# Optimization experiments

Hardware: AMD Instinct MI355X
Metric: run time of the kernel (lower is better)

The kernel has to match this reference:

```python
import jax, jax.numpy as jnp
import numpy as np

N = 50000
E = 800000
DIM = 128


def setup_inputs() -> dict:
    key = jax.random.key(0)
    ks = jax.random.split(key, 12)
    s = 1.0 / np.sqrt(DIM)
    s2 = 1.0 / np.sqrt(2 * DIM)
    return {
        "h": jax.random.normal(ks[0], (N, DIM), dtype=jnp.float32),
        "edge_index": jax.random.randint(ks[1], (2, E), 0, N, dtype=jnp.int64),
        # msg_mlp: Linear(dim,dim) -> ReLU -> Linear(dim,dim) -> ReLU
        "W1": jax.random.uniform(ks[2], (DIM, DIM), jnp.float32, -s, s),
        "b1": jax.random.uniform(ks[3], (DIM,), jnp.float32, -s, s),
        "W2": jax.random.uniform(ks[4], (DIM, DIM), jnp.float32, -s, s),
        "b2": jax.random.uniform(ks[5], (DIM,), jnp.float32, -s, s),
        # update_mlp: Linear(2*dim,dim) -> ReLU -> Linear(dim,dim)
        "U1": jax.random.uniform(ks[6], (2 * DIM, DIM), jnp.float32, -s2, s2),
        "c1": jax.random.uniform(ks[7], (DIM,), jnp.float32, -s2, s2),
        "U2": jax.random.uniform(ks[8], (DIM, DIM), jnp.float32, -s, s),
        "c2": jax.random.uniform(ks[9], (DIM,), jnp.float32, -s, s),
    }


def reference(h, edge_index, W1, b1, W2, b2, U1, c1, U2, c2):
    row, col = edge_index[0], edge_index[1]
    # gather source features and run message MLP on edges: [E, dim]
    x = h[col]
    m = jax.nn.relu(x @ W1 + b1)
    m = jax.nn.relu(m @ W2 + b2)
    # scatter-add messages to destination nodes: [N, dim]
    agg = jax.ops.segment_sum(m, row, num_segments=h.shape[0])
    # degree normalization (bincount of row, clamped at 1)
    deg = jax.ops.segment_sum(jnp.ones((m.shape[0],), m.dtype), row, num_segments=h.shape[0])
    deg = jnp.maximum(deg, 1.0)[:, None]
    agg = agg / deg
    # update MLP on [h, agg]
    z = jnp.concatenate([h, agg], axis=1)
    z = jax.nn.relu(z @ U1 + c1)
    return z @ U2 + c2
```

## Files before the change

### kernel.cpp

```cpp
#include <hip/hip_runtime.h>
#include <cstddef>

#define NN 50000
#define EE 800000
#define DIM 128
#define CAP 128

#define PREP_BLKS 320
#define ZERO_BLKS 49
#define EDGE_BLKS 3125
#define MLP_BLKS  782
#define GUP_BLKS  3125

typedef __attribute__((ext_vector_type(8))) short bf16x8;
typedef __attribute__((ext_vector_type(4))) float f32x4;

__device__ __forceinline__ unsigned short f2bf(float x) {
    unsigned u = __float_as_uint(x);
    unsigned r = (u + 0x7FFFu + ((u >> 16) & 1u)) >> 16;
    return (unsigned short)r;
}

__device__ __forceinline__ float bf2f(unsigned short b) {
    return __uint_as_float((unsigned)b << 16);
}

__device__ __forceinline__ int load_idx(const void* ei, bool i64, long long i) {
    return i64 ? (int)((const long long*)ei)[i] : ((const int*)ei)[i];
}

__device__ __forceinline__ bool detect_i64_inline(const void* ei) {
    int l = threadIdx.x & 63;
    int v = ((const int*)ei)[2 * l + 1];
    return __ballot(v != 0) == 0ULL;
}

__global__ __launch_bounds__(256) void prep_zero_kernel(
    const float* __restrict__ W1, const float* __restrict__ W2,
    const float* __restrict__ U1, const float* __restrict__ U2,
    unsigned short* __restrict__ W1t, unsigned short* __restrict__ W2t,
    unsigned short* __restrict__ U1h, unsigned short* __restrict__ U1l,
    unsigned short* __restrict__ U2h, unsigned short* __restrict__ U2l,
    int* __restrict__ cnt)
{
    int bid = blockIdx.x;
    if (bid < PREP_BLKS) {
        int idx = bid * 256 + threadIdx.x;
        if (idx < 32768) {
            int m   = idx >> 14;
            int rem = idx & 16383;
            int n = rem >> 7, k = rem & 127;
            const float* W = m ? W2 : W1;
            unsigned short* Wt = m ? W2t : W1t;
            Wt[n * DIM + k] = f2bf(W[k * DIM + n]);
        } else if (idx < 65536) {
            int r = idx - 32768;
            int k = r >> 7, n = r & 127;
            float w = U1[r];
            unsigned short hx = f2bf(w);
            U1h[n * 256 + k] = hx;
            U1l[n * 256 + k] = f2bf(w - bf2f(hx));
        } else {
            int r = idx - 65536;
            int k = r >> 7, n = r & 127;
            float w = U2[r];
            unsigned short hx = f2bf(w);
            U2h[n * 128 + k] = hx;
            U2l[n * 128 + k] = f2bf(w - bf2f(hx));
        }
    } else {
        int base = (bid - PREP_BLKS) * 1024 + threadIdx.x * 4;
        if (base + 4 <= NN) {
            *(int4*)(cnt + base) = (int4){0, 0, 0, 0};
        } else {
            #pragma unroll
            for (int k = 0; k < 4; ++k)
                if (base + k < NN) cnt[base + k] = 0;
        }
    }
}

__global__ __launch_bounds__(256) void bucket_mlp_kernel(
    const void* __restrict__ ei, const float* __restrict__ h,
    const unsigned short* __restrict__ W1t, const float* __restrict__ b1,
    const unsigned short* __restrict__ W2t, const float* __restrict__ b2,
    int* __restrict__ cnt, int* __restrict__ bucket,
    unsigned short* __restrict__ Mh)
{
    __shared__ unsigned short xs[4][16][136];

    if (blockIdx.x < EDGE_BLKS) {
        bool i64 = detect_i64_inline(ei);
        int e = blockIdx.x * 256 + threadIdx.x;
        if (e < EE) {
            int r = load_idx(ei, i64, e);
            int c = load_idx(ei, i64, (long long)EE + e);
            int slot = atomicAdd(&cnt[r], 1);
            if (slot < CAP) bucket[r * CAP + slot] = c;
        }
        return;
    }

    const int tid  = threadIdx.x;
    const int lane = tid & 63;
    const int wid  = tid >> 6;
    const int g    = lane >> 4;
    const int c    = lane & 15;
    const int half = lane >> 5;
    const int hl   = lane & 31;
    const int nbase = (blockIdx.x - EDGE_BLKS) * 64 + wid * 16;

    #pragma unroll
    for (int e = 0; e < 16; e += 2) {
        int n = nbase + e + half;
        int nc = n < NN ? n : NN - 1;
        float4 v = *(const float4*)(h + (size_t)nc * DIM + hl * 4);
        unsigned short h0 = f2bf(v.x), h1 = f2bf(v.y), h2 = f2bf(v.z), h3 = f2bf(v.w);
        *(uint2*)&xs[wid][e + half][hl * 4] =
            (uint2){(unsigned)h0 | ((unsigned)h1 << 16), (unsigned)h2 | ((unsigned)h3 << 16)};
    }

    bf16x8 a[4];
    #pragma unroll
    for (int s = 0; s < 4; ++s)
        a[s] = *(const bf16x8*)&xs[wid][c][s * 32 + g * 8];

    f32x4 acc[8];
    #pragma unroll
    for (int t = 0; t < 8; ++t) {
        float bv = b1[t * 16 + c];
        acc[t] = (f32x4){bv, bv, bv, bv};
    }
    #pragma unroll
    for (int t = 0; t < 8; ++t) {
        #pragma unroll
        for (int s = 0; s < 4; ++s) {
            bf16x8 bf = *(const bf16x8*)&W1t[(t * 16 + c) * DIM + s * 32 + g * 8];
            acc[t] = __builtin_amdgcn_mfma_f32_16x16x32_bf16(a[s], bf, acc[t], 0, 0, 0);
        }
    }
    #pragma unroll
    for (int t = 0; t < 8; ++t)
        #pragma unroll
        for (int j = 0; j < 4; ++j)
            xs[wid][g * 4 + j][t * 16 + c] = f2bf(fmaxf(acc[t][j], 0.f));

    #pragma unroll
    for (int s = 0; s < 4; ++s)
        a[s] = *(const bf16x8*)&xs[wid][c][s * 32 + g * 8];

    #pragma unroll
    for (int t = 0; t < 8; ++t) {
        float bv = b2[t * 16 + c];
        acc[t] = (f32x4){bv, bv, bv, bv};
    }
    #pragma unroll
    for (int t = 0; t < 8; ++t) {
        #pragma unroll
        for (int s = 0; s < 4; ++s) {
            bf16x8 bf = *(const bf16x8*)&W2t[(t * 16 + c) * DIM + s * 32 + g * 8];
            acc[t] = __builtin_amdgcn_mfma_f32_16x16x32_bf16(a[s], bf, acc[t], 0, 0, 0);
        }
    }

    #pragma unroll
    for (int t = 0; t < 8; ++t)
        #pragma unroll
        for (int j = 0; j < 4; ++j)
            xs[wid][g * 4 + j][t * 16 + c] = f2bf(fmaxf(acc[t][j], 0.f));

    #pragma unroll
    for (int e = 0; e < 16; ++e) {
        int n = nbase + e;
        if (n < NN)
            *(unsigned*)(Mh + (size_t)n * DIM + lane * 2) = *(const unsigned*)&xs[wid][e][lane * 2];
    }
}

__global__ __launch_bounds__(256, 8) void gup4_kernel(
    const float* __restrict__ h,
    const unsigned short* __restrict__ Mh, const int* __restrict__ bucket,
    const int* __restrict__ cnt,
    const unsigned short* __restrict__ U1h, const unsigned short* __restrict__ U1l,
    const unsigned short* __restrict__ U2h, const unsigned short* __restrict__ U2l,
    const float* __restrict__ c1, const float* __restrict__ c2,
    float* __restrict__ out)
{
    __shared__ unsigned short xa[2][16][136];
    __shared__ unsigned short xh[2][16][136];
    const int tid  = threadIdx.x;
    const int lane = tid & 63;
    const int wid  = tid >> 6;
    const int g    = lane >> 4;
    const int c    = lane & 15;
    const int half = lane >> 5;
    const int hl   = lane & 31;
    const int nbase = blockIdx.x * 16;

    #pragma unroll 1
    for (int pass = 0; pass < 2; ++pass) {
        int r  = 4 * wid + 2 * pass + half;
        int n  = nbase + r;
        int d  = cnt[n];
        int dg = d < CAP ? d : CAP;
        const int* brow = bucket + (size_t)n * CAP;
        float s0 = 0.f, s1 = 0.f, s2 = 0.f, s3 = 0.f;
        #pragma unroll 1
        for (int base = 0; base < dg; base += 32) {
            int m = dg - base; if (m > 32) m = 32;
            int idx = (hl < m) ? brow[base + hl] : 0;
            int j = 0;
            for (; j + 8 <= m; j += 8) {
                uint2 u[8];
                #pragma unroll
                for (int k = 0; k < 8; ++k) {
                    int si = __shfl(idx, (half << 5) + j + k);
                    u[k] = *(const uint2*)(Mh + (size_t)si * DIM + hl * 4);
                }
                #pragma unroll
                for (int k = 0; k < 8; ++k) {
                    s0 += __uint_as_float(u[k].x << 16);
                    s1 += __uint_as_float(u[k].x & 0xFFFF0000u);
                    s2 += __uint_as_float(u[k].y << 16);
                    s3 += __uint_as_float(u[k].y & 0xFFFF0000u);
                }
            }
            for (; j < m; ++j) {
                int si = __shfl(idx, (half << 5) + j);
                uint2 u0 = *(const uint2*)(Mh + (size_t)si * DIM + hl * 4);
                s0 += __uint_as_float(u0.x << 16);
                s1 += __uint_as_float(u0.x & 0xFFFF0000u);
                s2 += __uint_as_float(u0.y << 16);
                s3 += __uint_as_float(u0.y & 0xFFFF0000u);
            }
        }
        float inv = 1.0f / fmaxf((float)d, 1.0f);
        s0 *= inv; s1 *= inv; s2 *= inv; s3 *= inv;
        unsigned short h0 = f2bf(s0), h1 = f2bf(s1), h2 = f2bf(s2), h3 = f2bf(s3);
        unsigned short l0 = f2bf(s0 - bf2f(h0)), l1 = f2bf(s1 - bf2f(h1));
        unsigned short l2 = f2bf(s2 - bf2f(h2)), l3 = f2bf(s3 - bf2f(h3));
        *(uint2*)&xa[0][r][hl * 4] =
            (uint2){(unsigned)h0 | ((unsigned)h1 << 16), (unsigned)h2 | ((unsigned)h3 << 16)};
        *(uint2*)&xa[1][r][hl * 4] =
            (uint2){(unsigned)l0 | ((unsigned)l1 << 16), (unsigned)l2 | ((unsigned)l3 << 16)};

        float4 v = *(const float4*)(h + (size_t)n * DIM + hl * 4);
        unsigned short p0 = f2bf(v.x), p1 = f2bf(v.y), p2 = f2bf(v.z), p3 = f2bf(v.w);
        unsigned short q0 = f2bf(v.x - bf2f(p0)), q1 = f2bf(v.y - bf2f(p1));
        unsigned short q2 = f2bf(v.z - bf2f(p2)), q3 = f2bf(v.w - bf2f(p3));
        *(uint2*)&xh[0][r][hl * 4] =
            (uint2){(unsigned)p0 | ((unsigned)p1 << 16), (unsigned)p2 | ((unsigned)p3 << 16)};
        *(uint2*)&xh[1][r][hl * 4] =
            (uint2){(unsigned)q0 | ((unsigned)q1 << 16), (unsigned)q2 | ((unsigned)q3 << 16)};
    }
    __syncthreads();

    f32x4 acc[2];
    #pragma unroll
    for (int tt = 0; tt < 2; ++tt) {
        int t = 2 * wid + tt;
        float bv = c1[t * 16 + c];
        acc[tt] = (f32x4){bv, bv, bv, bv};
    }
    {
        bf16x8 ah[4], al[4];
        #pragma unroll
        for (int s = 0; s < 4; ++s) {
            ah[s] = *(const bf16x8*)&xa[0][c][s * 32 + g * 8];
            al[s] = *(const bf16x8*)&xa[1][c][s * 32 + g * 8];
        }
        #pragma unroll
        for (int tt = 0; tt < 2; ++tt) {
            int t = 2 * wid + tt;
            #pragma unroll
            for (int s = 0; s < 4; ++s) {
                int kof = 128 + s * 32 + g * 8;
                bf16x8 bh = *(const bf16x8*)&U1h[(t * 16 + c) * 256 + kof];
                bf16x8 bl = *(const bf16x8*)&U1l[(t * 16 + c) * 256 + kof];
                acc[tt] = __builtin_amdgcn_mfma_f32_16x16x32_bf16(ah[s], bh, acc[tt], 0, 0, 0);
                acc[tt] = __builtin_amdgcn_mfma_f32_16x16x32_bf16(al[s], bh, acc[tt], 0, 0, 0);
                acc[tt] = __builtin_amdgcn_mfma_f32_16x16x32_bf16(ah[s], bl, acc[tt], 0, 0, 0);
            }
        }
        #pragma unroll
        for (int s = 0; s < 4; ++s) {
            ah[s] = *(const bf16x8*)&xh[0][c][s * 32 + g * 8];
            al[s] = *(const bf16x8*)&xh[1][c][s * 32 + g * 8];
        }
        #pragma unroll
        for (int tt = 0; tt < 2; ++tt) {
            int t = 2 * wid + tt;
            #pragma unroll
            for (int s = 0; s < 4; ++s) {
                int kof = s * 32 + g * 8;
                bf16x8 bh = *(const bf16x8*)&U1h[(t * 16 + c) * 256 + kof];
                bf16x8 bl = *(const bf16x8*)&U1l[(t * 16 + c) * 256 + kof];
                acc[tt] = __builtin_amdgcn_mfma_f32_16x16x32_bf16(ah[s], bh, acc[tt], 0, 0, 0);
                acc[tt] = __builtin_amdgcn_mfma_f32_16x16x32_bf16(al[s], bh, acc[tt], 0, 0, 0);
                acc[tt] = __builtin_amdgcn_mfma_f32_16x16x32_bf16(ah[s], bl, acc[tt], 0, 0, 0);
            }
        }
    }
    __syncthreads();

    #pragma unroll
    for (int tt = 0; tt < 2; ++tt) {
        int t = 2 * wid + tt;
        #pragma unroll
        for (int j = 0; j < 4; ++j) {
            float yv = fmaxf(acc[tt][j], 0.f);
            unsigned short hx = f2bf(yv);
            xh[0][g * 4 + j][t * 16 + c] = hx;
            xh[1][g * 4 + j][t * 16 + c] = f2bf(yv - bf2f(hx));
        }
    }
    __syncthreads();

    bf16x8 yh[4], yl[4];
    #pragma unroll
    for (int s = 0; s < 4; ++s) {
        yh[s] = *(const bf16x8*)&xh[0][c][s * 32 + g * 8];
        yl[s] = *(const bf16x8*)&xh[1][c][s * 32 + g * 8];
    }
    f32x4 acc2[2];
    #pragma unroll
    for (int tt = 0; tt < 2; ++tt) {
        int t = 2 * wid + tt;
        float bv = c2[t * 16 + c];
        acc2[tt] = (f32x4){bv, bv, bv, bv};
    }
    #pragma unroll
    for (int tt = 0; tt < 2; ++tt) {
        int t = 2 * wid + tt;
        #pragma unroll
        for (int s = 0; s < 4; ++s) {
            int kof = s * 32 + g * 8;
            bf16x8 bh = *(const bf16x8*)&U2h[(t * 16 + c) * 128 + kof];
            bf16x8 bl = *(const bf16x8*)&U2l[(t * 16 + c) * 128 + kof];
            acc2[tt] = __builtin_amdgcn_mfma_f32_16x16x32_bf16(yh[s], bh, acc2[tt], 0, 0, 0);
            acc2[tt] = __builtin_amdgcn_mfma_f32_16x16x32_bf16(yl[s], bh, acc2[tt], 0, 0, 0);
            acc2[tt] = __builtin_amdgcn_mfma_f32_16x16x32_bf16(yh[s], bl, acc2[tt], 0, 0, 0);
        }
    }

    #pragma unroll
    for (int tt = 0; tt < 2; ++tt) {
        int t = 2 * wid + tt;
        #pragma unroll
        for (int j = 0; j < 4; ++j) {
            int n = nbase + g * 4 + j;
            out[(size_t)n * DIM + t * 16 + c] = acc2[tt][j];
        }
    }
}

__global__ void detect_i64_kernel(const int* __restrict__ ei, int* __restrict__ flag) {
    int l = threadIdx.x;
    int v = ei[2 * l + 1];
    unsigned long long b = __ballot(v != 0);
    if (l == 0) flag[0] = (b == 0ULL) ? 1 : 0;
}

__global__ __launch_bounds__(256) void prep_w_kernel(
    const float* __restrict__ W1, const float* __restrict__ W2,
    unsigned short* __restrict__ W1t, unsigned short* __restrict__ W2t)
{
    int idx = blockIdx.x * 256 + threadIdx.x;
    int m   = idx >> 14;
    int rem = idx & 16383;
    int n = rem >> 7, k = rem & 127;
    const float* W = m ? W2 : W1;
    unsigned short* Wt = m ? W2t : W1t;
    Wt[n * DIM + k] = f2bf(W[k * DIM + n]);
}

__global__ __launch_bounds__(256) void deg_i_kernel(const void* __restrict__ ei,
                                                    const int* __restrict__ flag,
                                                    int* __restrict__ deg) {
    bool i64 = flag[0] != 0;
    int e = blockIdx.x * 256 + threadIdx.x;
    if (e < EE) {
        int r = load_idx(ei, i64, e);
        atomicAdd(&deg[r], 1);
    }
}

__global__ __launch_bounds__(256) void msg_kernel(
    const float* __restrict__ h, const void* __restrict__ ei, const int* __restrict__ flag,
    const unsigned short* __restrict__ W1t, const float* __restrict__ b1,
    const unsigned short* __restrict__ W2t, const float* __restrict__ b2,
    float* __restrict__ agg)
{
    __shared__ unsigned short xs[4][16][136];
    const int tid  = threadIdx.x;
    const int lane = tid & 63;
    const int wid  = tid >> 6;
    const int g    = lane >> 4;
    const int c    = lane & 15;
    const bool i64 = flag[0] != 0;
    const int ebase = blockIdx.x * 64 + wid * 16;

    #pragma unroll
    for (int e = 0; e < 16; ++e) {
        int src = load_idx(ei, i64, (long long)EE + (ebase + e));
        float2 v = *(const float2*)(h + (size_t)src * DIM + lane * 2);
        unsigned p = (unsigned)f2bf(v.x) | ((unsigned)f2bf(v.y) << 16);
        *(unsigned*)&xs[wid][e][lane * 2] = p;
    }
    __syncthreads();

    bf16x8 a[4];
    #pragma unroll
    for (int s = 0; s < 4; ++s)
        a[s] = *(const bf16x8*)&xs[wid][c][s * 32 + g * 8];

    f32x4 acc[8];
    #pragma unroll
    for (int t = 0; t < 8; ++t) {
        float bv = b1[t * 16 + c];
        acc[t] = (f32x4){bv, bv, bv, bv};
    }
    #pragma unroll
    for (int t = 0; t < 8; ++t) {
        #pragma unroll
        for (int s = 0; s < 4; ++s) {
            bf16x8 bf = *(const bf16x8*)&W1t[(t * 16 + c) * DIM + s * 32 + g * 8];
            acc[t] = __builtin_amdgcn_mfma_f32_16x16x32_bf16(a[s], bf, acc[t], 0, 0, 0);
        }
    }
    __syncthreads();
    #pragma unroll
    for (int t = 0; t < 8; ++t)
        #pragma unroll
        for (int j = 0; j < 4; ++j)
            xs[wid][g * 4 + j][t * 16 + c] = f2bf(fmaxf(acc[t][j], 0.f));
    __syncthreads();

    #pragma unroll
    for (int s = 0; s < 4; ++s)
        a[s] = *(const bf16x8*)&xs[wid][c][s * 32 + g * 8];

    #pragma unroll
    for (int t = 0; t < 8; ++t) {
        float bv = b2[t * 16 + c];
        acc[t] = (f32x4){bv, bv, bv, bv};
    }
    #pragma unroll
    for (int t = 0; t < 8; ++t) {
        #pragma unroll
        for (int s = 0; s < 4; ++s) {
            bf16x8 bf = *(const bf16x8*)&W2t[(t * 16 + c) * DIM + s * 32 + g * 8];
            acc[t] = __builtin_amdgcn_mfma_f32_16x16x32_bf16(a[s], bf, acc[t], 0, 0, 0);
        }
    }

    #pragma unroll
    for (int j = 0; j < 4; ++j) {
        int r = load_idx(ei, i64, ebase + g * 4 + j);
        #pragma unroll
        for (int t = 0; t < 8; ++t)
            atomicAdd(&agg[(size_t)r * DIM + t * 16 + c], fmaxf(acc[t][j], 0.f));
    }
}

__global__ __launch_bounds__(256) void upd_kernel(
    const float* __restrict__ h, const float* __restrict__ aggout,
    const int* __restrict__ deg,
    const float* __restrict__ U1, const float* __restrict__ c1,
    const float* __restrict__ U2, const float* __restrict__ c2,
    float* __restrict__ out)
{
    __shared__ float zs[4][8][2 * DIM];
    const int tid  = threadIdx.x;
    const int lane = tid & 63;
    const int wid  = tid >> 6;
    const int nbase = blockIdx.x * 32 + wid * 8;

    #pragma unroll
    for (int i = 0; i < 8; ++i) {
        int n = nbase + i;
        if (n < NN) {
            float2 hv = *(const float2*)(h + (size_t)n * DIM + lane * 2);
            *(float2*)&zs[wid][i][lane * 2] = hv;
            float d = fmaxf((float)deg[n], 1.0f);
            float inv = 1.0f / d;
            float2 av = *(const float2*)(aggout + (size_t)n * DIM + lane * 2);
            av.x *= inv; av.y *= inv;
            *(float2*)&zs[wid][i][DIM + lane * 2] = av;
        }
    }
    __syncthreads();

    float acc0[8], acc1[8];
    {
        float cc0 = c1[lane], cc1 = c1[lane + 64];
        #pragma unroll
        for (int i = 0; i < 8; ++i) { acc0[i] = cc0; acc1[i] = cc1; }
    }
    for (int k = 0; k < 2 * DIM; k += 4) {
        float wa[4], wb[4];
        #pragma unroll
        for (int kk = 0; kk < 4; ++kk) {
            wa[kk] = U1[(k + kk) * DIM + lane];
            wb[kk] = U1[(k + kk) * DIM + lane + 64];
        }
        #pragma unroll
        for (int i = 0; i < 8; ++i) {
            float4 zv = *(const float4*)&zs[wid][i][k];
            acc0[i] = fmaf(zv.x, wa[0], acc0[i]);
            acc1[i] = fmaf(zv.x, wb[0], acc1[i]);
            acc0[i] = fmaf(zv.y, wa[1], acc0[i]);
            acc1[i] = fmaf(zv.y, wb[1], acc1[i]);
            acc0[i] = fmaf(zv.z, wa[2], acc0[i]);
            acc1[i] = fmaf(zv.z, wb[2], acc1[i]);
            acc0[i] = fmaf(zv.w, wa[3], acc0[i]);
            acc1[i] = fmaf(zv.w, wb[3], acc1[i]);
        }
    }
    __syncthreads();
    #pragma unroll
    for (int i = 0; i < 8; ++i) {
        zs[wid][i][lane]      = fmaxf(acc0[i], 0.f);
        zs[wid][i][lane + 64] = fmaxf(acc1[i], 0.f);
    }
    __syncthreads();

    {
        float cc0 = c2[lane], cc1 = c2[lane + 64];
        #pragma unroll
        for (int i = 0; i < 8; ++i) { acc0[i] = cc0; acc1[i] = cc1; }
    }
    for (int k = 0; k < DIM; k += 4) {
        float wa[4], wb[4];
        #pragma unroll
        for (int kk = 0; kk < 4; ++kk) {
            wa[kk] = U2[(k + kk) * DIM + lane];
            wb[kk] = U2[(k + kk) * DIM + lane + 64];
        }
        #pragma unroll
        for (int i = 0; i < 8; ++i) {
            float4 zv = *(const float4*)&zs[wid][i][k];
            acc0[i] = fmaf(zv.x, wa[0], acc0[i]);
            acc1[i] = fmaf(zv.x, wb[0], acc1[i]);
            acc0[i] = fmaf(zv.y, wa[1], acc0[i]);
            acc1[i] = fmaf(zv.y, wb[1], acc1[i]);
            acc0[i] = fmaf(zv.z, wa[2], acc0[i]);
            acc1[i] = fmaf(zv.z, wb[2], acc1[i]);
            acc0[i] = fmaf(zv.w, wa[3], acc0[i]);
            acc1[i] = fmaf(zv.w, wb[3], acc1[i]);
        }
    }

    #pragma unroll
    for (int i = 0; i < 8; ++i) {
        int n = nbase + i;
        if (n < NN) {
            out[(size_t)n * DIM + lane]      = acc0[i];
            out[(size_t)n * DIM + lane + 64] = acc1[i];
        }
    }
}

extern "C" void kernel_launch(void* const* d_in, const int* in_sizes, int n_in,
                              void* d_out, int out_size, void* d_ws, size_t ws_size,
                              hipStream_t stream) {
    const float* h  = (const float*)d_in[0];
    const void*  ei = d_in[1];
    const float* W1 = (const float*)d_in[2];
    const float* b1 = (const float*)d_in[3];
    const float* W2 = (const float*)d_in[4];
    const float* b2 = (const float*)d_in[5];
    const float* U1 = (const float*)d_in[6];
    const float* c1 = (const float*)d_in[7];
    const float* U2 = (const float*)d_in[8];
    const float* c2 = (const float*)d_in[9];
    float* out = (float*)d_out;

    const size_t BIG_BYTES = 38862144;
    const bool big = ws_size >= BIG_BYTES;

    char* wsb = (char*)d_ws;
    unsigned short *Mh, *W1t, *W2t, *U1h, *U1l, *U2h, *U2l;
    int *bucket, *cnt, *flag;
    if (big) {
        Mh     = (unsigned short*)wsb;
        bucket = (int*)(wsb + 12800000);
        cnt    = (int*)(wsb + 38400000);
        flag   = nullptr;
        W1t    = (unsigned short*)(wsb + 38600000);
        W2t    = (unsigned short*)(wsb + 38632768);
        U1h    = (unsigned short*)(wsb + 38665536);
        U1l    = (unsigned short*)(wsb + 38731072);
        U2h    = (unsigned short*)(wsb + 38796608);
        U2l    = (unsigned short*)(wsb + 38829376);
    } else {
        Mh     = nullptr; bucket = nullptr;
        U1h = U1l = U2h = U2l = nullptr;
        cnt    = (int*)wsb;
        flag   = (int*)(wsb + 200000);
        W1t    = (unsigned short*)(wsb + 200064);
        W2t    = (unsigned short*)(wsb + 200064 + 32768);
    }

    if (big) {
        prep_zero_kernel<<<PREP_BLKS + ZERO_BLKS, 256, 0, stream>>>(
            W1, W2, U1, U2, W1t, W2t, U1h, U1l, U2h, U2l, cnt);
        bucket_mlp_kernel<<<EDGE_BLKS + MLP_BLKS, 256, 0, stream>>>(
            ei, h, W1t, b1, W2t, b2, cnt, bucket, Mh);
        gup4_kernel<<<GUP_BLKS, 256, 0, stream>>>(h, Mh, bucket, cnt,
                                                  U1h, U1l, U2h, U2l, c1, c2, out);
    } else {
        detect_i64_kernel<<<1, 64, 0, stream>>>((const int*)ei, flag);
        prep_w_kernel<<<128, 256, 0, stream>>>(W1, W2, W1t, W2t);
        hipMemsetAsync(cnt, 0, (size_t)NN * sizeof(int), stream);
        deg_i_kernel<<<(EE + 255) / 256, 256, 0, stream>>>(ei, flag, cnt);
        hipMemsetAsync(d_out, 0, (size_t)NN * DIM * sizeof(float), stream);
        msg_kernel<<<EE / 64, 256, 0, stream>>>(h, ei, flag, W1t, b1, W2t, b2, out);
        upd_kernel<<<(NN + 31) / 32, 256, 0, stream>>>(h, out, cnt, U1, c1, U2, c2, out);
    }
}
```

Baseline: 200.7 us.

## Split edge buckets into eight sub-buckets per node to reduce atomic contention

The edge bucketing now spreads each node's counter and bucket across eight groups, chosen by edge block index, so concurrent atomicAdds on the same row counter are spread over eight addresses. Bucket writes use nontemporal stores. The aggregation kernel sums the eight group counts with shuffles and walks each sub-bucket in turn. The cost is a larger workspace (more counters to zero), up to eight smaller, less efficient gather loops per node, and a per-group cap of 32 that could drop edges if a group overflows. Falls back to the small path if the workspace is below the new threshold.

```diff
diff --git a/kernel.cpp b/kernel.cpp
--- a/kernel.cpp
+++ b/kernel.cpp
@@ -4,10 +4,11 @@
 #define NN 50000
 #define EE 800000
 #define DIM 128
-#define CAP 128
+#define NG 8
+#define CAPG 32
 
 #define PREP_BLKS 320
-#define ZERO_BLKS 49
+#define ZERO_BLKS 391
 #define EDGE_BLKS 3125
 #define MLP_BLKS  782
 #define GUP_BLKS  3125
@@ -41,7 +42,7 @@
     unsigned short* __restrict__ W1t, unsigned short* __restrict__ W2t,
     unsigned short* __restrict__ U1h, unsigned short* __restrict__ U1l,
     unsigned short* __restrict__ U2h, unsigned short* __restrict__ U2l,
-    int* __restrict__ cnt)
+    int* __restrict__ cnt8)
 {
     int bid = blockIdx.x;
     if (bid < PREP_BLKS) {
@@ -70,12 +71,12 @@
         }
     } else {
         int base = (bid - PREP_BLKS) * 1024 + threadIdx.x * 4;
-        if (base + 4 <= NN) {
-            *(int4*)(cnt + base) = (int4){0, 0, 0, 0};
+        if (base + 4 <= NG * NN) {
+            *(int4*)(cnt8 + base) = (int4){0, 0, 0, 0};
         } else {
             #pragma unroll
             for (int k = 0; k < 4; ++k)
-                if (base + k < NN) cnt[base + k] = 0;
+                if (base + k < NG * NN) cnt8[base + k] = 0;
         }
     }
 }
@@ -84,7 +85,7 @@
     const void* __restrict__ ei, const float* __restrict__ h,
     const unsigned short* __restrict__ W1t, const float* __restrict__ b1,
     const unsigned short* __restrict__ W2t, const float* __restrict__ b2,
-    int* __restrict__ cnt, int* __restrict__ bucket,
+    int* __restrict__ cnt8, int* __restrict__ bucket8,
     unsigned short* __restrict__ Mh)
 {
     __shared__ unsigned short xs[4][16][136];
@@ -92,11 +93,13 @@
     if (blockIdx.x < EDGE_BLKS) {
         bool i64 = detect_i64_inline(ei);
         int e = blockIdx.x * 256 + threadIdx.x;
+        int g = blockIdx.x & (NG - 1);
         if (e < EE) {
             int r = load_idx(ei, i64, e);
             int c = load_idx(ei, i64, (long long)EE + e);
-            int slot = atomicAdd(&cnt[r], 1);
-            if (slot < CAP) bucket[r * CAP + slot] = c;
+            int slot = atomicAdd(&cnt8[g * NN + r], 1);
+            if (slot < CAPG)
+                __builtin_nontemporal_store(c, &bucket8[((size_t)g * NN + r) * CAPG + slot]);
         }
         return;
     }
@@ -179,8 +182,8 @@
 
 __global__ __launch_bounds__(256, 8) void gup4_kernel(
     const float* __restrict__ h,
-    const unsigned short* __restrict__ Mh, const int* __restrict__ bucket,
-    const int* __restrict__ cnt,
+    const unsigned short* __restrict__ Mh, const int* __restrict__ bucket8,
+    const int* __restrict__ cnt8,
     const unsigned short* __restrict__ U1h, const unsigned short* __restrict__ U1l,
     const unsigned short* __restrict__ U2h, const unsigned short* __restrict__ U2l,
     const float* __restrict__ c1, const float* __restrict__ c2,
@@ -195,26 +198,31 @@
     const int c    = lane & 15;
     const int half = lane >> 5;
     const int hl   = lane & 31;
+    const int hb   = half << 5;
     const int nbase = blockIdx.x * 16;
 
     #pragma unroll 1
     for (int pass = 0; pass < 2; ++pass) {
         int r  = 4 * wid + 2 * pass + half;
         int n  = nbase + r;
-        int d  = cnt[n];
-        int dg = d < CAP ? d : CAP;
-        const int* brow = bucket + (size_t)n * CAP;
+        int cv = (hl < NG) ? cnt8[hl * NN + n] : 0;
+        int d = 0;
+        #pragma unroll
+        for (int gg = 0; gg < NG; ++gg) d += __shfl(cv, hb + gg);
+
         float s0 = 0.f, s1 = 0.f, s2 = 0.f, s3 = 0.f;
         #pragma unroll 1
-        for (int base = 0; base < dg; base += 32) {
-            int m = dg - base; if (m > 32) m = 32;
-            int idx = (hl < m) ? brow[base + hl] : 0;
+        for (int gg = 0; gg < NG; ++gg) {
+            int dg = __shfl(cv, hb + gg);
+            int dgc = dg < CAPG ? dg : CAPG;
+            const int* brow = bucket8 + ((size_t)gg * NN + n) * CAPG;
+            int idx = (hl < dgc) ? brow[hl] : 0;
             int j = 0;
-            for (; j + 8 <= m; j += 8) {
+            for (; j + 8 <= dgc; j += 8) {
                 uint2 u[8];
                 #pragma unroll
                 for (int k = 0; k < 8; ++k) {
-                    int si = __shfl(idx, (half << 5) + j + k);
+                    int si = __shfl(idx, hb + j + k);
                     u[k] = *(const uint2*)(Mh + (size_t)si * DIM + hl * 4);
                 }
                 #pragma unroll
@@ -225,8 +233,8 @@
                     s3 += __uint_as_float(u[k].y & 0xFFFF0000u);
                 }
             }
-            for (; j < m; ++j) {
-                int si = __shfl(idx, (half << 5) + j);
+            for (; j < dgc; ++j) {
+                int si = __shfl(idx, hb + j);
                 uint2 u0 = *(const uint2*)(Mh + (size_t)si * DIM + hl * 4);
                 s0 += __uint_as_float(u0.x << 16);
                 s1 += __uint_as_float(u0.x & 0xFFFF0000u);
@@ -576,46 +584,46 @@
     const float* c2 = (const float*)d_in[9];
     float* out = (float*)d_out;
 
-    const size_t BIG_BYTES = 38862144;
+    const size_t BIG_BYTES = 65862144;
     const bool big = ws_size >= BIG_BYTES;
 
     char* wsb = (char*)d_ws;
     unsigned short *Mh, *W1t, *W2t, *U1h, *U1l, *U2h, *U2l;
-    int *bucket, *cnt, *flag;
+    int *bucket8, *cnt8, *flag;
     if (big) {
-        Mh     = (unsigned short*)wsb;
-        bucket = (int*)(wsb + 12800000);
-        cnt    = (int*)(wsb + 38400000);
-        flag   = nullptr;
-        W1t    = (unsigned short*)(wsb + 38600000);
-        W2t    = (unsigned short*)(wsb + 38632768);
-        U1h    = (unsigned short*)(wsb + 38665536);
-        U1l    = (unsigned short*)(wsb + 38731072);
-        U2h    = (unsigned short*)(wsb + 38796608);
-        U2l    = (unsigned short*)(wsb + 38829376);
+        Mh      = (unsigned short*)wsb;
+        bucket8 = (int*)(wsb + 12800000);
+        cnt8    = (int*)(wsb + 64000000);
+        flag    = nullptr;
+        W1t     = (unsigned short*)(wsb + 65600000);
+        W2t     = (unsigned short*)(wsb + 65632768);
+        U1h     = (unsigned short*)(wsb + 65665536);
+        U1l     = (unsigned short*)(wsb + 65731072);
+        U2h     = (unsigned short*)(wsb + 65796608);
+        U2l     = (unsigned short*)(wsb + 65829376);
     } else {
-        Mh     = nullptr; bucket = nullptr;
+        Mh      = nullptr; bucket8 = nullptr;
         U1h = U1l = U2h = U2l = nullptr;
-        cnt    = (int*)wsb;
-        flag   = (int*)(wsb + 200000);
-        W1t    = (unsigned short*)(wsb + 200064);
-        W2t    = (unsigned short*)(wsb + 200064 + 32768);
+        cnt8    = (int*)wsb;
+        flag    = (int*)(wsb + 200000);
+        W1t     = (unsigned short*)(wsb + 200064);
+        W2t     = (unsigned short*)(wsb + 200064 + 32768);
     }
 
     if (big) {
         prep_zero_kernel<<<PREP_BLKS + ZERO_BLKS, 256, 0, stream>>>(
-            W1, W2, U1, U2, W1t, W2t, U1h, U1l, U2h, U2l, cnt);
+            W1, W2, U1, U2, W1t, W2t, U1h, U1l, U2h, U2l, cnt8);
         bucket_mlp_kernel<<<EDGE_BLKS + MLP_BLKS, 256, 0, stream>>>(
-            ei, h, W1t, b1, W2t, b2, cnt, bucket, Mh);
-        gup4_kernel<<<GUP_BLKS, 256, 0, stream>>>(h, Mh, bucket, cnt,
+            ei, h, W1t, b1, W2t, b2, cnt8, bucket8, Mh);
+        gup4_kernel<<<GUP_BLKS, 256, 0, stream>>>(h, Mh, bucket8, cnt8,
                                                   U1h, U1l, U2h, U2l, c1, c2, out);
     } else {
         detect_i64_kernel<<<1, 64, 0, stream>>>((const int*)ei, flag);
         prep_w_kernel<<<128, 256, 0, stream>>>(W1, W2, W1t, W2t);
-        hipMemsetAsync(cnt, 0, (size_t)NN * sizeof(int), stream);
-        deg_i_kernel<<<(EE + 255) / 256, 256, 0, stream>>>(ei, flag, cnt);
+        hipMemsetAsync(cnt8, 0, (size_t)NN * sizeof(int), stream);
+        deg_i_kernel<<<(EE + 255) / 256, 256, 0, stream>>>(ei, flag, cnt8);
         hipMemsetAsync(d_out, 0, (size_t)NN * DIM * sizeof(float), stream);
         msg_kernel<<<EE / 64, 256, 0, stream>>>(h, ei, flag, W1t, b1, W2t, b2, out);
-        upd_kernel<<<(NN + 31) / 32, 256, 0, stream>>>(h, out, cnt, U1, c1, U2, c2, out);
-    }
-}
+        upd_kernel<<<(NN + 31) / 32, 256, 0, stream>>>(h, out, cnt8, U1, c1, U2, c2, out);
+    }
+}
```

After: 244.2 us. +21.7%, slower.

## Pad degree counters, use nontemporal bucket stores, split node MLP across waves

Applied to the files above, without the earlier changes.

Degree counters are padded to a 64-byte stride so atomics on different nodes no longer contend on the same cache line. Bucket writes use nontemporal stores. The node message MLP now has each block process 16 nodes, with the four waves splitting the output columns and synchronising through shared memory. This cuts per-wave registers and LDS, giving more blocks and occupancy. The cost is a 16x larger counter array to zero, a larger workspace requirement, and extra block barriers.

```diff
diff --git a/kernel.cpp b/kernel.cpp
--- a/kernel.cpp
+++ b/kernel.cpp
@@ -5,11 +5,12 @@
 #define EE 800000
 #define DIM 128
 #define CAP 128
+#define CSTRIDE 16
 
 #define PREP_BLKS 320
-#define ZERO_BLKS 49
+#define ZERO_BLKS 782
 #define EDGE_BLKS 3125
-#define MLP_BLKS  782
+#define MLP2_BLKS 3125
 #define GUP_BLKS  3125
 
 typedef __attribute__((ext_vector_type(8))) short bf16x8;
@@ -41,7 +42,7 @@
     unsigned short* __restrict__ W1t, unsigned short* __restrict__ W2t,
     unsigned short* __restrict__ U1h, unsigned short* __restrict__ U1l,
     unsigned short* __restrict__ U2h, unsigned short* __restrict__ U2l,
-    int* __restrict__ cnt)
+    int* __restrict__ cnt16)
 {
     int bid = blockIdx.x;
     if (bid < PREP_BLKS) {
@@ -70,24 +71,24 @@
         }
     } else {
         int base = (bid - PREP_BLKS) * 1024 + threadIdx.x * 4;
-        if (base + 4 <= NN) {
-            *(int4*)(cnt + base) = (int4){0, 0, 0, 0};
+        if (base + 4 <= CSTRIDE * NN) {
+            *(int4*)(cnt16 + base) = (int4){0, 0, 0, 0};
         } else {
             #pragma unroll
             for (int k = 0; k < 4; ++k)
-                if (base + k < NN) cnt[base + k] = 0;
-        }
-    }
-}
-
-__global__ __launch_bounds__(256) void bucket_mlp_kernel(
+                if (base + k < CSTRIDE * NN) cnt16[base + k] = 0;
+        }
+    }
+}
+
+__global__ __launch_bounds__(256, 8) void bucket_mlp_kernel(
     const void* __restrict__ ei, const float* __restrict__ h,
     const unsigned short* __restrict__ W1t, const float* __restrict__ b1,
     const unsigned short* __restrict__ W2t, const float* __restrict__ b2,
-    int* __restrict__ cnt, int* __restrict__ bucket,
+    int* __restrict__ cnt16, int* __restrict__ bucket,
     unsigned short* __restrict__ Mh)
 {
-    __shared__ unsigned short xs[4][16][136];
+    __shared__ unsigned short xs[16][136];
 
     if (blockIdx.x < EDGE_BLKS) {
         bool i64 = detect_i64_inline(ei);
@@ -95,8 +96,9 @@
         if (e < EE) {
             int r = load_idx(ei, i64, e);
             int c = load_idx(ei, i64, (long long)EE + e);
-            int slot = atomicAdd(&cnt[r], 1);
-            if (slot < CAP) bucket[r * CAP + slot] = c;
+            int slot = atomicAdd(&cnt16[(size_t)r * CSTRIDE], 1);
+            if (slot < CAP)
+                __builtin_nontemporal_store(c, &bucket[(size_t)r * CAP + slot]);
         }
         return;
     }
@@ -108,79 +110,91 @@
     const int c    = lane & 15;
     const int half = lane >> 5;
     const int hl   = lane & 31;
-    const int nbase = (blockIdx.x - EDGE_BLKS) * 64 + wid * 16;
-
-    #pragma unroll
-    for (int e = 0; e < 16; e += 2) {
-        int n = nbase + e + half;
-        int nc = n < NN ? n : NN - 1;
-        float4 v = *(const float4*)(h + (size_t)nc * DIM + hl * 4);
+    const int nbase = (blockIdx.x - EDGE_BLKS) * 16;
+
+    #pragma unroll
+    for (int pass = 0; pass < 2; ++pass) {
+        int r = 4 * wid + 2 * pass + half;
+        int n = nbase + r;
+        float4 v = *(const float4*)(h + (size_t)n * DIM + hl * 4);
         unsigned short h0 = f2bf(v.x), h1 = f2bf(v.y), h2 = f2bf(v.z), h3 = f2bf(v.w);
-        *(uint2*)&xs[wid][e + half][hl * 4] =
+        *(uint2*)&xs[r][hl * 4] =
             (uint2){(unsigned)h0 | ((unsigned)h1 << 16), (unsigned)h2 | ((unsigned)h3 << 16)};
     }
+    __syncthreads();
 
     bf16x8 a[4];
     #pragma unroll
     for (int s = 0; s < 4; ++s)
-        a[s] = *(const bf16x8*)&xs[wid][c][s * 32 + g * 8];
-
-    f32x4 acc[8];
-    #pragma unroll
-    for (int t = 0; t < 8; ++t) {
+        a[s] = *(const bf16x8*)&xs[c][s * 32 + g * 8];
+    __syncthreads();
+
+    f32x4 acc[2];
+    #pragma unroll
+    for (int tt = 0; tt < 2; ++tt) {
+        int t = 2 * wid + tt;
         float bv = b1[t * 16 + c];
-        acc[t] = (f32x4){bv, bv, bv, bv};
-    }
-    #pragma unroll
-    for (int t = 0; t < 8; ++t) {
+        acc[tt] = (f32x4){bv, bv, bv, bv};
+    }
+    #pragma unroll
+    for (int tt = 0; tt < 2; ++tt) {
+        int t = 2 * wid + tt;
         #pragma unroll
         for (int s = 0; s < 4; ++s) {
             bf16x8 bf = *(const bf16x8*)&W1t[(t * 16 + c) * DIM + s * 32 + g * 8];
-            acc[t] = __builtin_amdgcn_mfma_f32_16x16x32_bf16(a[s], bf, acc[t], 0, 0, 0);
-        }
-    }
-    #pragma unroll
-    for (int t = 0; t < 8; ++t)
+            acc[tt] = __builtin_amdgcn_mfma_f32_16x16x32_bf16(a[s], bf, acc[tt], 0, 0, 0);
+        }
+    }
+    #pragma unroll
+    for (int tt = 0; tt < 2; ++tt) {
+        int t = 2 * wid + tt;
         #pragma unroll
         for (int j = 0; j < 4; ++j)
-            xs[wid][g * 4 + j][t * 16 + c] = f2bf(fmaxf(acc[t][j], 0.f));
+            xs[g * 4 + j][t * 16 + c] = f2bf(fmaxf(acc[tt][j], 0.f));
+    }
+    __syncthreads();
 
     #pragma unroll
     for (int s = 0; s < 4; ++s)
-        a[s] = *(const bf16x8*)&xs[wid][c][s * 32 + g * 8];
-
-    #pragma unroll
-    for (int t = 0; t < 8; ++t) {
+        a[s] = *(const bf16x8*)&xs[c][s * 32 + g * 8];
+    __syncthreads();
+
+    #pragma unroll
+    for (int tt = 0; tt < 2; ++tt) {
+        int t = 2 * wid + tt;
         float bv = b2[t * 16 + c];
-        acc[t] = (f32x4){bv, bv, bv, bv};
-    }
-    #pragma unroll
-    for (int t = 0; t < 8; ++t) {
+        acc[tt] = (f32x4){bv, bv, bv, bv};
+    }
+    #pragma unroll
+    for (int tt = 0; tt < 2; ++tt) {
+        int t = 2 * wid + tt;
         #pragma unroll
         for (int s = 0; s < 4; ++s) {
             bf16x8 bf = *(const bf16x8*)&W2t[(t * 16 + c) * DIM + s * 32 + g * 8];
-            acc[t] = __builtin_amdgcn_mfma_f32_16x16x32_bf16(a[s], bf, acc[t], 0, 0, 0);
-        }
-    }
-
-    #pragma unroll
-    for (int t = 0; t < 8; ++t)
+            acc[tt] = __builtin_amdgcn_mfma_f32_16x16x32_bf16(a[s], bf, acc[tt], 0, 0, 0);
+        }
+    }
+    #pragma unroll
+    for (int tt = 0; tt < 2; ++tt) {
+        int t = 2 * wid + tt;
         #pragma unroll
         for (int j = 0; j < 4; ++j)
-            xs[wid][g * 4 + j][t * 16 + c] = f2bf(fmaxf(acc[t][j], 0.f));
-
-    #pragma unroll
-    for (int e = 0; e < 16; ++e) {
-        int n = nbase + e;
-        if (n < NN)
-            *(unsigned*)(Mh + (size_t)n * DIM + lane * 2) = *(const unsigned*)&xs[wid][e][lane * 2];
+            xs[g * 4 + j][t * 16 + c] = f2bf(fmaxf(acc[tt][j], 0.f));
+    }
+    __syncthreads();
+
+    #pragma unroll
+    for (int e = 0; e < 4; ++e) {
+        int r = wid * 4 + e;
+        int n = nbase + r;
+        *(unsigned*)(Mh + (size_t)n * DIM + lane * 2) = *(const unsigned*)&xs[r][lane * 2];
     }
 }
 
 __global__ __launch_bounds__(256, 8) void gup4_kernel(
     const float* __restrict__ h,
     const unsigned short* __restrict__ Mh, const int* __restrict__ bucket,
-    const int* __restrict__ cnt,
+    const int* __restrict__ cnt16,
     const unsigned short* __restrict__ U1h, const unsigned short* __restrict__ U1l,
     const unsigned short* __restrict__ U2h, const unsigned short* __restrict__ U2l,
     const float* __restrict__ c1, const float* __restrict__ c2,
@@ -195,13 +209,14 @@
     const int c    = lane & 15;
     const int half = lane >> 5;
     const int hl   = lane & 31;
+    const int hb   = half << 5;
     const int nbase = blockIdx.x * 16;
 
     #pragma unroll 1
     for (int pass = 0; pass < 2; ++pass) {
         int r  = 4 * wid + 2 * pass + half;
         int n  = nbase + r;
-        int d  = cnt[n];
+        int d  = cnt16[(size_t)n * CSTRIDE];
         int dg = d < CAP ? d : CAP;
         const int* brow = bucket + (size_t)n * CAP;
         float s0 = 0.f, s1 = 0.f, s2 = 0.f, s3 = 0.f;
@@ -214,7 +229,7 @@
                 uint2 u[8];
                 #pragma unroll
                 for (int k = 0; k < 8; ++k) {
-                    int si = __shfl(idx, (half << 5) + j + k);
+                    int si = __shfl(idx, hb + j + k);
                     u[k] = *(const uint2*)(Mh + (size_t)si * DIM + hl * 4);
                 }
                 #pragma unroll
@@ -226,7 +241,7 @@
                 }
             }
             for (; j < m; ++j) {
-                int si = __shfl(idx, (half << 5) + j);
+                int si = __shfl(idx, hb + j);
                 uint2 u0 = *(const uint2*)(Mh + (size_t)si * DIM + hl * 4);
                 s0 += __uint_as_float(u0.x << 16);
                 s1 += __uint_as_float(u0.x & 0xFFFF0000u);
@@ -576,27 +591,27 @@
     const float* c2 = (const float*)d_in[9];
     float* out = (float*)d_out;
 
-    const size_t BIG_BYTES = 38862144;
+    const size_t BIG_BYTES = 41862144;
     const bool big = ws_size >= BIG_BYTES;
 
     char* wsb = (char*)d_ws;
     unsigned short *Mh, *W1t, *W2t, *U1h, *U1l, *U2h, *U2l;
-    int *bucket, *cnt, *flag;
+    int *bucket, *cnt16, *flag;
     if (big) {
         Mh     = (unsigned short*)wsb;
         bucket = (int*)(wsb + 12800000);
-        cnt    = (int*)(wsb + 38400000);
+        cnt16  = (int*)(wsb + 38400000);
         flag   = nullptr;
-        W1t    = (unsigned short*)(wsb + 38600000);
-        W2t    = (unsigned short*)(wsb + 38632768);
-        U1h    = (unsigned short*)(wsb + 38665536);
-        U1l    = (unsigned short*)(wsb + 38731072);
-        U2h    = (unsigned short*)(wsb + 38796608);
-        U2l    = (unsigned short*)(wsb + 38829376);
+        W1t    = (unsigned short*)(wsb + 41600000);
+        W2t    = (unsigned short*)(wsb + 41632768);
+        U1h    = (unsigned short*)(wsb + 41665536);
+        U1l    = (unsigned short*)(wsb + 41731072);
+        U2h    = (unsigned short*)(wsb + 41796608);
+        U2l    = (unsigned short*)(wsb + 41829376);
     } else {
         Mh     = nullptr; bucket = nullptr;
         U1h = U1l = U2h = U2l = nullptr;
-        cnt    = (int*)wsb;
+        cnt16  = (int*)wsb;
         flag   = (int*)(wsb + 200000);
         W1t    = (unsigned short*)(wsb + 200064);
         W2t    = (unsigned short*)(wsb + 200064 + 32768);
@@ -604,18 +619,18 @@
 
     if (big) {
         prep_zero_kernel<<<PREP_BLKS + ZERO_BLKS, 256, 0, stream>>>(
-            W1, W2, U1, U2, W1t, W2t, U1h, U1l, U2h, U2l, cnt);
-        bucket_mlp_kernel<<<EDGE_BLKS + MLP_BLKS, 256, 0, stream>>>(
-            ei, h, W1t, b1, W2t, b2, cnt, bucket, Mh);
-        gup4_kernel<<<GUP_BLKS, 256, 0, stream>>>(h, Mh, bucket, cnt,
+            W1, W2, U1, U2, W1t, W2t, U1h, U1l, U2h, U2l, cnt16);
+        bucket_mlp_kernel<<<EDGE_BLKS + MLP2_BLKS, 256, 0, stream>>>(
+            ei, h, W1t, b1, W2t, b2, cnt16, bucket, Mh);
+        gup4_kernel<<<GUP_BLKS, 256, 0, stream>>>(h, Mh, bucket, cnt16,
                                                   U1h, U1l, U2h, U2l, c1, c2, out);
     } else {
         detect_i64_kernel<<<1, 64, 0, stream>>>((const int*)ei, flag);
         prep_w_kernel<<<128, 256, 0, stream>>>(W1, W2, W1t, W2t);
-        hipMemsetAsync(cnt, 0, (size_t)NN * sizeof(int), stream);
-        deg_i_kernel<<<(EE + 255) / 256, 256, 0, stream>>>(ei, flag, cnt);
+        hipMemsetAsync(cnt16, 0, (size_t)NN * sizeof(int), stream);
+        deg_i_kernel<<<(EE + 255) / 256, 256, 0, stream>>>(ei, flag, cnt16);
         hipMemsetAsync(d_out, 0, (size_t)NN * DIM * sizeof(float), stream);
         msg_kernel<<<EE / 64, 256, 0, stream>>>(h, ei, flag, W1t, b1, W2t, b2, out);
-        upd_kernel<<<(NN + 31) / 32, 256, 0, stream>>>(h, out, cnt, U1, c1, U2, c2, out);
-    }
-}
+        upd_kernel<<<(NN + 31) / 32, 256, 0, stream>>>(h, out, cnt16, U1, c1, U2, c2, out);
+    }
+}
```

New measurement: 180.8 us, median of 2. -9.9%, faster.
